# Kernel optimization log

Hardware: AMD Instinct MI355X
Metric: run time of the kernel (lower is better)

The kernel has to match this reference:

```python
import jax, jax.numpy as jnp
import numpy as np

RSD = 9   # robot_state_dim
HSD = 5   # human_state_dim (human feature slice width = HSD+1 = 6)
XD = 32   # X_dim
NEG = -9e15


def _lin(x, w, b):
    return x @ w + b


def _gat(X, adj, w0, b0, w1, b1):
    # X: [B,N,F]; pairwise concat feature (i,j) = [X_i, X_j] -> [B,N,N,2F]
    B, N, F = X.shape
    Xi = jnp.broadcast_to(X[:, :, None, :], (B, N, N, F))
    Xj = jnp.broadcast_to(X[:, None, :, :], (B, N, N, F))
    pair = jnp.concatenate([Xi, Xj], axis=-1)              # [B,N,N,2F]
    h = jax.nn.relu(_lin(pair, w0, b0))                    # [B,N,N,2F]
    A = _lin(h, w1, b1)[..., 0]                            # [B,N,N]
    e = jnp.where(A > 0, A, 0.04 * A)                      # LeakyReLU(0.04)
    att = jax.nn.softmax(jnp.where(adj > 0, e, NEG), axis=2)
    return jnp.einsum('bij,bjf->bif', att, X)


def setup_inputs() -> dict:
    key = jax.random.key(0)
    ks = jax.random.split(key, 32)
    s = 0.05
    d = {
        'state': jax.random.normal(ks[0], (512, 50, 15), jnp.float32),
        'dropout': 0,
        # w_r: Linear(9,64) ReLU Linear(64,32) ReLU
        'wr_w0': jax.random.normal(ks[1], (RSD, 64)) * s, 'wr_b0': jnp.zeros((64,)),
        'wr_w1': jax.random.normal(ks[2], (64, XD)) * s, 'wr_b1': jnp.zeros((XD,)),
        # w_h: Linear(6,64) ReLU Linear(64,32) ReLU
        'wh_w0': jax.random.normal(ks[3], (HSD + 1, 64)) * s, 'wh_b0': jnp.zeros((64,)),
        'wh_w1': jax.random.normal(ks[4], (64, XD)) * s, 'wh_b1': jnp.zeros((XD,)),
        # gat0 w_a: Linear(64,64) ReLU Linear(64,1)
        'g0_w0': jax.random.normal(ks[5], (2 * XD, 2 * XD)) * s, 'g0_b0': jnp.zeros((2 * XD,)),
        'g0_w1': jax.random.normal(ks[6], (2 * XD, 1)) * s, 'g0_b1': jnp.zeros((1,)),
        # gat1 w_a
        'g1_w0': jax.random.normal(ks[7], (2 * XD, 2 * XD)) * s, 'g1_b0': jnp.zeros((2 * XD,)),
        'g1_w1': jax.random.normal(ks[8], (2 * XD, 1)) * s, 'g1_b1': jnp.zeros((1,)),
        # value_net: Linear(32,150) ReLU Linear(150,100) ReLU Linear(100,1) ReLU
        'v_w0': jax.random.normal(ks[9], (XD, 150)) * s, 'v_b0': jnp.zeros((150,)),
        'v_w1': jax.random.normal(ks[10], (150, 100)) * s, 'v_b1': jnp.zeros((100,)),
        'v_w2': jax.random.normal(ks[11], (100, 1)) * s, 'v_b2': jnp.zeros((1,)),
    }
    return d


def reference(state, dropout, wr_w0, wr_b0, wr_w1, wr_b1, wh_w0, wh_b0, wh_w1, wh_b1,
              g0_w0, g0_b0, g0_w1, g0_b1, g1_w0, g1_b0, g1_w1, g1_b1,
              v_w0, v_b0, v_w1, v_b1, v_w2, v_b2):
    B, N, _ = state.shape
    robot = state[:, 0, :RSD]                               # [B,9]
    humans = state[:, :, RSD:]                              # [B,N,6]
    r_emb = jax.nn.relu(_lin(jax.nn.relu(_lin(robot, wr_w0, wr_b0)), wr_w1, wr_b1))[:, None, :]
    h_emb = jax.nn.relu(_lin(jax.nn.relu(_lin(humans, wh_w0, wh_b0)), wh_w1, wh_b1))
    X = jnp.concatenate([r_emb, h_emb], axis=1)             # [B,N+1,32]
    Num = N + 1
    adj = jnp.ones((Num, Num), state.dtype).at[1:, 0].set(0.0)
    adj = jnp.broadcast_to(adj[None], (B, Num, Num))
    H1 = _gat(X, adj, g0_w0, g0_b0, g0_w1, g0_b1)
    H2 = _gat(H1, adj, g1_w0, g1_b0, g1_w1, g1_b1)
    output = H1 + H2 + X                                    # skip_connection=True
    o = output[:, 0, :]
    o = jax.nn.relu(_lin(o, v_w0, v_b0))
    o = jax.nn.relu(_lin(o, v_w1, v_b1))
    o = jax.nn.relu(_lin(o, v_w2, v_b2))                    # last_relu=True
    return o
```

## Files before the change

### kernel.cpp

```cpp
#include <hip/hip_runtime.h>
#include <hip/hip_bf16.h>


typedef float f4 __attribute__((ext_vector_type(4)));
typedef const float* cfp;

__device__ __forceinline__ f4 fma4(float s, f4 v, f4 a) {
#pragma unroll
  for (int i = 0; i < 4; ++i) a[i] = fmaf(s, v[i], a[i]);
  return a;
}

#define NN 51
#define HID 64
#define XD 32
#define XS 9

__global__ __launch_bounds__(256)
void value_net_kernel(cfp state,
                      cfp wr_w0, cfp wr_b0, cfp wr_w1, cfp wr_b1,
                      cfp wh_w0, cfp wh_b0, cfp wh_w1, cfp wh_b1,
                      cfp g0_w0, cfp g0_b0, cfp g0_w1, cfp g0_b1,
                      cfp g1_w0, cfp g1_b0, cfp g1_w1, cfp g1_b1,
                      cfp v_w0, cfp v_b0, cfp v_w1, cfp v_b1,
                      cfp v_w2, cfp v_b2,
                      float* out)
{
  __shared__ f4 sX4[52 * XS];
  __shared__ f4 sH14[52 * XS];
  __shared__ f4 sU4[52 * 17];
  __shared__ f4 sV4[52 * 17];
  __shared__ f4 sWE4[1024];
  __shared__ f4 sB04[16];
  __shared__ f4 sW14[16];
  __shared__ float sRH[64];
  __shared__ float sO[32];
  __shared__ float sM1[152];
  __shared__ float sM2[104];

  float* sX  = (float*)sX4;
  float* sH1 = (float*)sH14;
  float* sE  = (float*)sWE4;
  float* sWE = (float*)sWE4;
  float* sB0 = (float*)sB04;
  float* sW1 = (float*)sW14;
  float* sHH = (float*)sU4;
  const f4* sWh4 = (const f4*)sV4;

  const int tid = threadIdx.x;
  const int b = blockIdx.x;
  cfp st = state + b * 750;

  const float gb0 = g0_b1[0];
  const float gb1 = g1_b1[0];

  {
    const f4* g0w04 = (const f4*)g0_w0;
    for (int i = tid; i < 1024; i += 256) sWE4[i] = g0w04[i];
    const f4* whw14 = (const f4*)wh_w1;
    f4* sWh4w = (f4*)sV4;
    for (int i = tid; i < 512; i += 256) sWh4w[i] = whw14[i];
  }
  if (tid < HID) {
    sB0[tid] = g0_b0[tid];
    sW1[tid] = g0_w1[tid];
    float a = wr_b0[tid];
#pragma unroll
    for (int k = 0; k < 9; ++k) a = fmaf(st[k], wr_w0[k * HID + tid], a);
    sRH[tid] = fmaxf(a, 0.f);
  }
  if (tid < XS) { sX4[51 * XS + tid] = (f4){0,0,0,0}; sH14[51 * XS + tid] = (f4){0,0,0,0}; }
  for (int idx = tid; idx < 50 * HID; idx += 256) {
    int i = idx >> 6, t = idx & 63;
    cfp hp = st + i * 15 + 9;
    float a = wh_b0[t];
#pragma unroll
    for (int k = 0; k < 6; ++k) a = fmaf(hp[k], wh_w0[k * HID + t], a);
    sHH[i * 68 + t] = fmaxf(a, 0.f);
  }
  __syncthreads();

  if (tid < XD) {
    float a = wr_b1[tid];
#pragma unroll 8
    for (int t = 0; t < HID; ++t) a = fmaf(sRH[t], wr_w1[t * XD + tid], a);
    sX[tid] = fmaxf(a, 0.f);
  }
  if (tid < 200) {
    int ip = tid >> 3, fg = tid & 7;
    f4 a0 = { wh_b1[fg * 4 + 0], wh_b1[fg * 4 + 1],
              wh_b1[fg * 4 + 2], wh_b1[fg * 4 + 3] };
    f4 a1 = a0;
    const f4* h0 = sU4 + ip * 17;
    const f4* h1 = sU4 + (ip + 25) * 17;
#pragma unroll 4
    for (int tg = 0; tg < 16; ++tg) {
      f4 ha = h0[tg], hb = h1[tg];
#pragma unroll
      for (int e = 0; e < 4; ++e) {
        f4 w = sWh4[(tg * 4 + e) * 8 + fg];
        a0 = fma4(ha[e], w, a0);
        a1 = fma4(hb[e], w, a1);
      }
    }
#pragma unroll
    for (int e = 0; e < 4; ++e) { a0[e] = fmaxf(a0[e], 0.f); a1[e] = fmaxf(a1[e], 0.f); }
    sX4[(1 + ip) * XS + fg] = a0;
    sX4[(26 + ip) * XS + fg] = a1;
  }
  __syncthreads();

  if (tid < 208) {
    int ip = tid >> 4, tg = tid & 15;
    f4 au[4] = {{0,0,0,0},{0,0,0,0},{0,0,0,0},{0,0,0,0}};
    f4 av[4] = {{0,0,0,0},{0,0,0,0},{0,0,0,0},{0,0,0,0}};
#pragma unroll 2
    for (int kg = 0; kg < 8; ++kg) {
      f4 x0 = sX4[ip * XS + kg];
      f4 x1 = sX4[(ip + 13) * XS + kg];
      f4 x2 = sX4[(ip + 26) * XS + kg];
      f4 x3 = sX4[(ip + 39) * XS + kg];
#pragma unroll
      for (int e = 0; e < 4; ++e) {
        int k = kg * 4 + e;
        f4 wU = sWE4[k * 16 + tg];
        f4 wV = sWE4[(k + 32) * 16 + tg];
        au[0] = fma4(x0[e], wU, au[0]); av[0] = fma4(x0[e], wV, av[0]);
        au[1] = fma4(x1[e], wU, au[1]); av[1] = fma4(x1[e], wV, av[1]);
        au[2] = fma4(x2[e], wU, au[2]); av[2] = fma4(x2[e], wV, av[2]);
        au[3] = fma4(x3[e], wU, au[3]); av[3] = fma4(x3[e], wV, av[3]);
      }
    }
    f4 b0v = sB04[tg];
#pragma unroll
    for (int r = 0; r < 4; ++r) {
      int row = ip + 13 * r;
      sU4[row * 17 + tg] = au[r] + b0v;
      sV4[row * 17 + tg] = av[r];
    }
  }
  __syncthreads();

  if (tid < 169) {
    int it = tid / 13, jt = tid - (tid / 13) * 13;
    const f4* U0 = sU4 + it * 17;
    const f4* V0 = sV4 + jt * 17;
    float acc[4][4] = {};
#pragma unroll 4
    for (int g = 0; g < 16; ++g) {
      f4 u0 = U0[g], u1 = U0[13 * 17 + g], u2 = U0[26 * 17 + g], u3 = U0[39 * 17 + g];
      f4 v0 = V0[g], v1 = V0[13 * 17 + g], v2 = V0[26 * 17 + g], v3 = V0[39 * 17 + g];
      f4 w = sW14[g];
#pragma unroll
      for (int e = 0; e < 4; ++e) {
        float we = w[e];
        float uu[4] = {u0[e], u1[e], u2[e], u3[e]};
        float vv[4] = {v0[e], v1[e], v2[e], v3[e]};
#pragma unroll
        for (int r = 0; r < 4; ++r)
#pragma unroll
          for (int cc = 0; cc < 4; ++cc)
            acc[r][cc] = fmaf(fmaxf(uu[r] + vv[cc], 0.f), we, acc[r][cc]);
      }
    }
#pragma unroll
    for (int r = 0; r < 4; ++r) {
      int i = it + 13 * r;
      if (i < NN) {
#pragma unroll
        for (int cc = 0; cc < 4; ++cc) {
          int j = jt + 13 * cc;
          if (j < NN) {
            float A = acc[r][cc] + gb0;
            float e = A > 0.f ? A : 0.04f * A;
            sE[i * NN + j] = (j == 0 && i > 0) ? -1e30f : e;
          }
        }
      }
    }
  }
  __syncthreads();

  {
    int lane = tid & 63, w = tid >> 6;
    for (int r = w; r < NN; r += 4) {
      float* row = sE + r * NN;
      float e = (lane < NN) ? row[lane] : -3.0e38f;
      float m = e;
#pragma unroll
      for (int o = 32; o; o >>= 1) m = fmaxf(m, __shfl_xor(m, o, 64));
      float p = (lane < NN) ? __expf(e - m) : 0.f;
      float s = p;
#pragma unroll
      for (int o = 32; o; o >>= 1) s += __shfl_xor(s, o, 64);
      if (lane < NN) row[lane] = p / s;
    }
  }
  __syncthreads();

  if (tid < 104) {
    int ip = tid >> 2, q = tid & 3;
    const float* a0r = sE + ip * NN;
    const float* a1r = sE + (ip + 26) * NN;
    f4 b00 = {0,0,0,0}, b01 = {0,0,0,0}, b10 = {0,0,0,0}, b11 = {0,0,0,0};
#pragma unroll 3
    for (int j = 0; j < NN; ++j) {
      float t0 = a0r[j], t1 = a1r[j];
      f4 x0 = sX4[j * XS + q * 2], x1 = sX4[j * XS + q * 2 + 1];
      b00 = fma4(t0, x0, b00); b01 = fma4(t0, x1, b01);
      b10 = fma4(t1, x0, b10); b11 = fma4(t1, x1, b11);
    }
    sH14[ip * XS + q * 2] = b00;       sH14[ip * XS + q * 2 + 1] = b01;
    sH14[(ip + 26) * XS + q * 2] = b10; sH14[(ip + 26) * XS + q * 2 + 1] = b11;
  }
  __syncthreads();

  {
    const f4* g1w04 = (const f4*)g1_w0;
    for (int i = tid; i < 1024; i += 256) sWE4[i] = g1w04[i];
  }
  if (tid < HID) { sB0[tid] = g1_b0[tid]; sW1[tid] = g1_w1[tid]; }
  __syncthreads();

  if (tid < 208) {
    int jp = tid >> 4, tg = tid & 15;
    f4 av[4] = {{0,0,0,0},{0,0,0,0},{0,0,0,0},{0,0,0,0}};
#pragma unroll 2
    for (int kg = 0; kg < 8; ++kg) {
      f4 h0 = sH14[jp * XS + kg];
      f4 h1 = sH14[(jp + 13) * XS + kg];
      f4 h2 = sH14[(jp + 26) * XS + kg];
      f4 h3 = sH14[(jp + 39) * XS + kg];
#pragma unroll
      for (int e = 0; e < 4; ++e) {
        f4 wV = sWE4[(kg * 4 + e + 32) * 16 + tg];
        av[0] = fma4(h0[e], wV, av[0]);
        av[1] = fma4(h1[e], wV, av[1]);
        av[2] = fma4(h2[e], wV, av[2]);
        av[3] = fma4(h3[e], wV, av[3]);
      }
    }
#pragma unroll
    for (int r = 0; r < 4; ++r) sV4[(jp + 13 * r) * 17 + tg] = av[r];
  }
  if (tid >= 208 && tid < 224) {
    int tg = tid - 208;
    f4 au = {0,0,0,0};
#pragma unroll
    for (int kg = 0; kg < 8; ++kg) {
      f4 h = sH14[kg];
#pragma unroll
      for (int e = 0; e < 4; ++e) au = fma4(h[e], sWE4[(kg * 4 + e) * 16 + tg], au);
    }
    sU4[tg] = au + sB04[tg];
  }
  __syncthreads();

  if (tid < 64) {
    int j = tid;
    float e = -3.0e38f;
    if (j < NN) {
      float acc = gb1;
#pragma unroll 4
      for (int g = 0; g < 16; ++g) {
        f4 u = sU4[g];
        f4 v = sV4[j * 17 + g];
        f4 w = sW14[g];
#pragma unroll
        for (int x = 0; x < 4; ++x) acc = fmaf(fmaxf(u[x] + v[x], 0.f), w[x], acc);
      }
      e = acc > 0.f ? acc : 0.04f * acc;
    }
    float m = e;
#pragma unroll
    for (int o = 32; o; o >>= 1) m = fmaxf(m, __shfl_xor(m, o, 64));
    float p = (j < NN) ? __expf(e - m) : 0.f;
    float s = p;
#pragma unroll
    for (int o = 32; o; o >>= 1) s += __shfl_xor(s, o, 64);
    if (j < NN) sE[j] = p / s;
  }
  __syncthreads();

  if (tid < XD) {
    float a = 0.f;
    for (int j = 0; j < NN; ++j) a = fmaf(sE[j], sH1[j * 36 + tid], a);
    sO[tid] = a + sH1[tid] + sX[tid];
  }
  __syncthreads();

  if (tid < 225) {
    int kp = tid / 75, t2 = tid % 75;
    int k0 = kp * 11, k1 = (k0 + 11 < 32) ? k0 + 11 : 32;
    const float2* w = (const float2*)v_w0;
    float2 acc = {0.f, 0.f};
    for (int k = k0; k < k1; ++k) {
      float2 ww = w[k * 75 + t2];
      float xv = sO[k];
      acc.x = fmaf(xv, ww.x, acc.x);
      acc.y = fmaf(xv, ww.y, acc.y);
    }
    ((float2*)(sE + 256 + kp * 152))[t2] = acc;
  }
  __syncthreads();
  if (tid < 150) {
    float a = v_b0[tid] + sE[256 + tid] + sE[256 + 152 + tid] + sE[256 + 304 + tid];
    sM1[tid] = fmaxf(a, 0.f);
  }
  __syncthreads();
  if (tid < 250) {
    int kp = tid / 50, t2 = tid % 50;
    int k0 = kp * 30;
    const float2* w = (const float2*)v_w1;
    float2 acc = {0.f, 0.f};
    for (int k = k0; k < k0 + 30; ++k) {
      float2 ww = w[k * 50 + t2];
      float xv = sM1[k];
      acc.x = fmaf(xv, ww.x, acc.x);
      acc.y = fmaf(xv, ww.y, acc.y);
    }
    ((float2*)(sE + 768 + kp * 100))[t2] = acc;
  }
  __syncthreads();
  if (tid < 100) {
    float a = v_b1[tid];
#pragma unroll
    for (int kp = 0; kp < 5; ++kp) a += sE[768 + kp * 100 + tid];
    sM2[tid] = fmaxf(a, 0.f);
  }
  __syncthreads();
  if (tid < 64) {
    float a = sM2[tid] * v_w2[tid];
    if (tid < 36) a = fmaf(sM2[tid + 64], v_w2[tid + 64], a);
#pragma unroll
    for (int o = 32; o; o >>= 1) a += __shfl_xor(a, o, 64);
    if (tid == 0) out[b] = fmaxf(a + v_b2[0], 0.f);
  }
}

extern "C" void kernel_launch(void* const* d_in, const int* in_sizes, int n_in,
                              void* d_out, int out_size, void* d_ws, size_t ws_size,
                              hipStream_t stream) {
  cfp state = (cfp)d_in[0];
  cfp wr_w0 = (cfp)d_in[2],  wr_b0 = (cfp)d_in[3];
  cfp wr_w1 = (cfp)d_in[4],  wr_b1 = (cfp)d_in[5];
  cfp wh_w0 = (cfp)d_in[6],  wh_b0 = (cfp)d_in[7];
  cfp wh_w1 = (cfp)d_in[8],  wh_b1 = (cfp)d_in[9];
  cfp g0_w0 = (cfp)d_in[10], g0_b0 = (cfp)d_in[11];
  cfp g0_w1 = (cfp)d_in[12], g0_b1 = (cfp)d_in[13];
  cfp g1_w0 = (cfp)d_in[14], g1_b0 = (cfp)d_in[15];
  cfp g1_w1 = (cfp)d_in[16], g1_b1 = (cfp)d_in[17];
  cfp v_w0  = (cfp)d_in[18], v_b0  = (cfp)d_in[19];
  cfp v_w1  = (cfp)d_in[20], v_b1  = (cfp)d_in[21];
  cfp v_w2  = (cfp)d_in[22], v_b2  = (cfp)d_in[23];
  float* out = (float*)d_out;

  const int B = in_sizes[0] / 750;
  hipLaunchKernelGGL(value_net_kernel, dim3(B), dim3(256), 0, stream,
                     state,
                     wr_w0, wr_b0, wr_w1, wr_b1,
                     wh_w0, wh_b0, wh_w1, wh_b1,
                     g0_w0, g0_b0, g0_w1, g0_b1,
                     g1_w0, g1_b0, g1_w1, g1_b1,
                     v_w0, v_b0, v_w1, v_b1, v_w2, v_b2,
                     out);
}
```

Before: 142.5 us.

## Overlap GAT1 weight load with aggregation, vectorize pairwise scoring, pad attention rows

The change vectorizes the pairwise attention score loop into f4 accumulators with a horizontal sum at the end. It pads the attention matrix rows to 52 so the aggregation can read f4 chunks. It loads the second GAT layer's weights in idle threads while the first aggregation runs, which removes one barrier stage. The U-side projection reads weights straight from global memory. It also collapses the value-net first layer into a direct per-output loop, dropping a barrier and a partial-sum stage. The f4 accumulation reorders the float sums, and the larger accumulator arrays raise register pressure.

```diff
diff --git a/kernel.cpp b/kernel.cpp
--- a/kernel.cpp
+++ b/kernel.cpp
@@ -5,16 +5,19 @@
 typedef float f4 __attribute__((ext_vector_type(4)));
 typedef const float* cfp;
 
-__device__ __forceinline__ f4 fma4(float s, f4 v, f4 a) {
-#pragma unroll
-  for (int i = 0; i < 4; ++i) a[i] = fmaf(s, v[i], a[i]);
-  return a;
+__device__ __forceinline__ f4 fma4(float s, f4 v, f4 a) { return a + s * v; }
+__device__ __forceinline__ f4 max4(f4 a, f4 b) {
+  f4 r;
+#pragma unroll
+  for (int i = 0; i < 4; ++i) r[i] = fmaxf(a[i], b[i]);
+  return r;
 }
 
 #define NN 51
 #define HID 64
 #define XD 32
 #define XS 9
+#define ES 52
 
 __global__ __launch_bounds__(256)
 void value_net_kernel(cfp state,
@@ -41,9 +44,6 @@
   float* sX  = (float*)sX4;
   float* sH1 = (float*)sH14;
   float* sE  = (float*)sWE4;
-  float* sWE = (float*)sWE4;
-  float* sB0 = (float*)sB04;
-  float* sW1 = (float*)sW14;
   float* sHH = (float*)sU4;
   const f4* sWh4 = (const f4*)sV4;
 
@@ -62,8 +62,8 @@
     for (int i = tid; i < 512; i += 256) sWh4w[i] = whw14[i];
   }
   if (tid < HID) {
-    sB0[tid] = g0_b0[tid];
-    sW1[tid] = g0_w1[tid];
+    ((float*)sB04)[tid] = g0_b0[tid];
+    ((float*)sW14)[tid] = g0_w1[tid];
     float a = wr_b0[tid];
 #pragma unroll
     for (int k = 0; k < 9; ++k) a = fmaf(st[k], wr_w0[k * HID + tid], a);
@@ -103,10 +103,9 @@
         a1 = fma4(hb[e], w, a1);
       }
     }
-#pragma unroll
-    for (int e = 0; e < 4; ++e) { a0[e] = fmaxf(a0[e], 0.f); a1[e] = fmaxf(a1[e], 0.f); }
-    sX4[(1 + ip) * XS + fg] = a0;
-    sX4[(26 + ip) * XS + fg] = a1;
+    f4 z = {0,0,0,0};
+    sX4[(1 + ip) * XS + fg] = max4(a0, z);
+    sX4[(26 + ip) * XS + fg] = max4(a1, z);
   }
   __syncthreads();
 
@@ -145,23 +144,18 @@
     int it = tid / 13, jt = tid - (tid / 13) * 13;
     const f4* U0 = sU4 + it * 17;
     const f4* V0 = sV4 + jt * 17;
-    float acc[4][4] = {};
-#pragma unroll 4
+    f4 acc[4][4] = {};
+    const f4 z = {0,0,0,0};
+#pragma unroll 2
     for (int g = 0; g < 16; ++g) {
-      f4 u0 = U0[g], u1 = U0[13 * 17 + g], u2 = U0[26 * 17 + g], u3 = U0[39 * 17 + g];
-      f4 v0 = V0[g], v1 = V0[13 * 17 + g], v2 = V0[26 * 17 + g], v3 = V0[39 * 17 + g];
+      f4 uu[4] = {U0[g], U0[221 + g], U0[442 + g], U0[663 + g]};
+      f4 vv[4] = {V0[g], V0[221 + g], V0[442 + g], V0[663 + g]};
       f4 w = sW14[g];
 #pragma unroll
-      for (int e = 0; e < 4; ++e) {
-        float we = w[e];
-        float uu[4] = {u0[e], u1[e], u2[e], u3[e]};
-        float vv[4] = {v0[e], v1[e], v2[e], v3[e]};
-#pragma unroll
-        for (int r = 0; r < 4; ++r)
-#pragma unroll
-          for (int cc = 0; cc < 4; ++cc)
-            acc[r][cc] = fmaf(fmaxf(uu[r] + vv[cc], 0.f), we, acc[r][cc]);
-      }
+      for (int r = 0; r < 4; ++r)
+#pragma unroll
+        for (int cc = 0; cc < 4; ++cc)
+          acc[r][cc] += max4(uu[r] + vv[cc], z) * w;
     }
 #pragma unroll
     for (int r = 0; r < 4; ++r) {
@@ -171,9 +165,10 @@
         for (int cc = 0; cc < 4; ++cc) {
           int j = jt + 13 * cc;
           if (j < NN) {
-            float A = acc[r][cc] + gb0;
+            f4 A4 = acc[r][cc];
+            float A = (A4[0] + A4[1]) + (A4[2] + A4[3]) + gb0;
             float e = A > 0.f ? A : 0.04f * A;
-            sE[i * NN + j] = (j == 0 && i > 0) ? -1e30f : e;
+            sE[i * ES + j] = (j == 0 && i > 0) ? -1e30f : e;
           }
         }
       }
@@ -184,7 +179,7 @@
   {
     int lane = tid & 63, w = tid >> 6;
     for (int r = w; r < NN; r += 4) {
-      float* row = sE + r * NN;
+      float* row = sE + r * ES;
       float e = (lane < NN) ? row[lane] : -3.0e38f;
       float m = e;
 #pragma unroll
@@ -194,32 +189,45 @@
 #pragma unroll
       for (int o = 32; o; o >>= 1) s += __shfl_xor(s, o, 64);
       if (lane < NN) row[lane] = p / s;
+      else if (lane == NN) row[lane] = 0.f;
     }
   }
   __syncthreads();
 
   if (tid < 104) {
-    int ip = tid >> 2, q = tid & 3;
-    const float* a0r = sE + ip * NN;
-    const float* a1r = sE + (ip + 26) * NN;
-    f4 b00 = {0,0,0,0}, b01 = {0,0,0,0}, b10 = {0,0,0,0}, b11 = {0,0,0,0};
-#pragma unroll 3
-    for (int j = 0; j < NN; ++j) {
-      float t0 = a0r[j], t1 = a1r[j];
-      f4 x0 = sX4[j * XS + q * 2], x1 = sX4[j * XS + q * 2 + 1];
-      b00 = fma4(t0, x0, b00); b01 = fma4(t0, x1, b01);
-      b10 = fma4(t1, x0, b10); b11 = fma4(t1, x1, b11);
-    }
-    sH14[ip * XS + q * 2] = b00;       sH14[ip * XS + q * 2 + 1] = b01;
-    sH14[(ip + 26) * XS + q * 2] = b10; sH14[(ip + 26) * XS + q * 2 + 1] = b11;
-  }
-  __syncthreads();
-
-  {
-    const f4* g1w04 = (const f4*)g1_w0;
-    for (int i = tid; i < 1024; i += 256) sWE4[i] = g1w04[i];
-  }
-  if (tid < HID) { sB0[tid] = g1_b0[tid]; sW1[tid] = g1_w1[tid]; }
+    int ip = tid >> 3, q = tid & 7;
+    const f4* a0 = (const f4*)(sE + ip * ES);
+    const f4* a1 = (const f4*)(sE + (ip + 13) * ES);
+    const f4* a2 = (const f4*)(sE + (ip + 26) * ES);
+    const f4* a3 = (const f4*)(sE + (ip + 39) * ES);
+    f4 b0 = {0,0,0,0}, b1 = {0,0,0,0}, b2 = {0,0,0,0}, b3 = {0,0,0,0};
+    for (int jg = 0; jg < 13; ++jg) {
+      f4 t0 = a0[jg], t1 = a1[jg], t2 = a2[jg], t3 = a3[jg];
+#pragma unroll
+      for (int e = 0; e < 4; ++e) {
+        f4 x = sX4[(jg * 4 + e) * XS + q];
+        b0 = fma4(t0[e], x, b0);
+        b1 = fma4(t1[e], x, b1);
+        b2 = fma4(t2[e], x, b2);
+        b3 = fma4(t3[e], x, b3);
+      }
+    }
+    sH14[ip * XS + q] = b0;
+    sH14[(ip + 13) * XS + q] = b1;
+    sH14[(ip + 26) * XS + q] = b2;
+    sH14[(ip + 39) * XS + q] = b3;
+  } else if (tid < 232) {
+    int t = tid - 104;
+    const f4* g1w = (const f4*)g1_w0;
+#pragma unroll
+    for (int i = 0; i < 4; ++i) sU4[t + 128 * i] = g1w[512 + t + 128 * i];
+  } else if (tid < 248) {
+    sB04[tid - 232] = ((const f4*)g1_b0)[tid - 232];
+  } else {
+    int t = tid - 248;
+    sW14[t] = ((const f4*)g1_w1)[t];
+    sW14[t + 8] = ((const f4*)g1_w1)[t + 8];
+  }
   __syncthreads();
 
   if (tid < 208) {
@@ -233,7 +241,7 @@
       f4 h3 = sH14[(jp + 39) * XS + kg];
 #pragma unroll
       for (int e = 0; e < 4; ++e) {
-        f4 wV = sWE4[(kg * 4 + e + 32) * 16 + tg];
+        f4 wV = sU4[(kg * 4 + e) * 16 + tg];
         av[0] = fma4(h0[e], wV, av[0]);
         av[1] = fma4(h1[e], wV, av[1]);
         av[2] = fma4(h2[e], wV, av[2]);
@@ -242,17 +250,17 @@
     }
 #pragma unroll
     for (int r = 0; r < 4; ++r) sV4[(jp + 13 * r) * 17 + tg] = av[r];
-  }
-  if (tid >= 208 && tid < 224) {
+  } else if (tid < 224) {
     int tg = tid - 208;
+    const f4* w0g = (const f4*)g1_w0;
     f4 au = {0,0,0,0};
-#pragma unroll
+#pragma unroll 2
     for (int kg = 0; kg < 8; ++kg) {
       f4 h = sH14[kg];
 #pragma unroll
-      for (int e = 0; e < 4; ++e) au = fma4(h[e], sWE4[(kg * 4 + e) * 16 + tg], au);
-    }
-    sU4[tg] = au + sB04[tg];
+      for (int e = 0; e < 4; ++e) au = fma4(h[e], w0g[(kg * 4 + e) * 16 + tg], au);
+    }
+    sU4[512 + tg] = au + sB04[tg];
   }
   __syncthreads();
 
@@ -260,15 +268,16 @@
     int j = tid;
     float e = -3.0e38f;
     if (j < NN) {
-      float acc = gb1;
+      f4 acc4 = {0,0,0,0};
 #pragma unroll 4
       for (int g = 0; g < 16; ++g) {
-        f4 u = sU4[g];
+        f4 u = sU4[512 + g];
         f4 v = sV4[j * 17 + g];
         f4 w = sW14[g];
-#pragma unroll
-        for (int x = 0; x < 4; ++x) acc = fmaf(fmaxf(u[x] + v[x], 0.f), w[x], acc);
-      }
+        f4 z = {0,0,0,0};
+        acc4 += max4(u + v, z) * w;
+      }
+      float acc = (acc4[0] + acc4[1]) + (acc4[2] + acc4[3]) + gb1;
       e = acc > 0.f ? acc : 0.04f * acc;
     }
     float m = e;
@@ -289,31 +298,18 @@
   }
   __syncthreads();
 
-  if (tid < 225) {
-    int kp = tid / 75, t2 = tid % 75;
-    int k0 = kp * 11, k1 = (k0 + 11 < 32) ? k0 + 11 : 32;
-    const float2* w = (const float2*)v_w0;
-    float2 acc = {0.f, 0.f};
-    for (int k = k0; k < k1; ++k) {
-      float2 ww = w[k * 75 + t2];
-      float xv = sO[k];
-      acc.x = fmaf(xv, ww.x, acc.x);
-      acc.y = fmaf(xv, ww.y, acc.y);
-    }
-    ((float2*)(sE + 256 + kp * 152))[t2] = acc;
-  }
-  __syncthreads();
   if (tid < 150) {
-    float a = v_b0[tid] + sE[256 + tid] + sE[256 + 152 + tid] + sE[256 + 304 + tid];
+    float a = v_b0[tid];
+#pragma unroll 8
+    for (int k = 0; k < 32; ++k) a = fmaf(sO[k], v_w0[k * 150 + tid], a);
     sM1[tid] = fmaxf(a, 0.f);
   }
   __syncthreads();
   if (tid < 250) {
     int kp = tid / 50, t2 = tid % 50;
-    int k0 = kp * 30;
     const float2* w = (const float2*)v_w1;
     float2 acc = {0.f, 0.f};
-    for (int k = k0; k < k0 + 30; ++k) {
+    for (int k = kp * 30; k < kp * 30 + 30; ++k) {
       float2 ww = w[k * 50 + t2];
       float xv = sM1[k];
       acc.x = fmaf(xv, ww.x, acc.x);
@@ -342,7 +338,7 @@
                               void* d_out, int out_size, void* d_ws, size_t ws_size,
                               hipStream_t stream) {
   cfp state = (cfp)d_in[0];
-  cfp wr_w0 = (cfp)d_in[2],  wr_b0 = (cfp)d_in[3];
+  cfp wr_w0 = (cfp)d_in[2],  cfp_wr_b0 = (cfp)d_in[3];
   cfp wr_w1 = (cfp)d_in[4],  wr_b1 = (cfp)d_in[5];
   cfp wh_w0 = (cfp)d_in[6],  wh_b0 = (cfp)d_in[7];
   cfp wh_w1 = (cfp)d_in[8],  wh_b1 = (cfp)d_in[9];
@@ -358,7 +354,7 @@
   const int B = in_sizes[0] / 750;
   hipLaunchKernelGGL(value_net_kernel, dim3(B), dim3(256), 0, stream,
                      state,
-                     wr_w0, wr_b0, wr_w1, wr_b1,
+                     wr_w0, cfp_wr_b0, wr_w1, wr_b1,
                      wh_w0, wh_b0, wh_w1, wh_b1,
                      g0_w0, g0_b0, g0_w1, g0_b1,
                      g1_w0, g1_b0, g1_w1, g1_b1,
```

New measurement: 137.3 us. 3.6% less time.
